# Kernel tuning notes

Hardware: AMD Instinct MI355X
Metric: run time of the kernel (lower is better)

The kernel has to match this reference:

```python
import jax, jax.numpy as jnp
import numpy as np

B, H, K, T, OUT, NH = 512, 512, 6, 60, 2, 8

def _gelu(x):
    return jax.nn.gelu(x, approximate=False)  # torch nn.GELU default = exact erf

def _layernorm(x, g, b, eps=1e-5):
    m = jnp.mean(x, axis=-1, keepdims=True)
    v = jnp.var(x, axis=-1, keepdims=True)
    return (x - m) * jax.lax.rsqrt(v + eps) * g + b

def setup_inputs() -> dict:
    key = jax.random.key(0)
    ks = iter(jax.random.split(key, 40))
    def p(shape, scale=0.02):
        return jax.random.normal(next(ks), shape, dtype=jnp.float32) * scale
    return dict(
        interaction_ctx=p((B, H), 1.0),
        cooperative_ctx=p((B, H), 1.0),
        map_ctx=p((B, H), 1.0),
        mode_queries=p((K, H)),
        # context_proj: Linear(3H,H) -> GELU -> Linear(H,H)
        Wc1=p((3 * H, H)), bc1=jnp.zeros((H,), jnp.float32),
        Wc2=p((H, H)), bc2=jnp.zeros((H,), jnp.float32),
        # coarse_heads stacked over modes: Linear(H,2H)->GELU->Linear(2H,T*OUT)
        Wk1=p((K, H, 2 * H)), bk1=jnp.zeros((K, 2 * H), jnp.float32),
        Wk2=p((K, 2 * H, T * OUT)), bk2=jnp.zeros((K, T * OUT), jnp.float32),
        # traj_encoder: Linear(OUT,H)->GELU
        Wt=p((OUT, H)), bt=jnp.zeros((H,), jnp.float32),
        # refine_attn (MultiheadAttention) projections
        Wq_a=p((H, H)), bq_a=jnp.zeros((H,), jnp.float32),
        Wk_a=p((H, H)), bk_a=jnp.zeros((H,), jnp.float32),
        Wv_a=p((H, H)), bv_a=jnp.zeros((H,), jnp.float32),
        Wo_a=p((H, H)), bo_a=jnp.zeros((H,), jnp.float32),
        ln_g=jnp.ones((H,), jnp.float32), ln_b=jnp.zeros((H,), jnp.float32),
        # refine_heads stacked over modes: Linear(H,H)->GELU->Linear(H,OUT)
        Wr1=p((K, H, H)), br1=jnp.zeros((K, H), jnp.float32),
        Wr2=p((K, H, OUT)), br2=jnp.zeros((K, OUT), jnp.float32),
        # conf_head: Linear(H,64)->ReLU->Linear(64,1)
        Wf1=p((H, 64)), bf1=jnp.zeros((64,), jnp.float32),
        Wf2=p((64, 1)), bf2=jnp.zeros((1,), jnp.float32),
    )

def reference(interaction_ctx, cooperative_ctx, map_ctx, mode_queries,
              Wc1, bc1, Wc2, bc2, Wk1, bk1, Wk2, bk2, Wt, bt,
              Wq_a, bq_a, Wk_a, bk_a, Wv_a, bv_a, Wo_a, bo_a,
              ln_g, ln_b, Wr1, br1, Wr2, br2, Wf1, bf1, Wf2, bf2):
    # dropout layers are identity in eval mode
    combined = jnp.concatenate([interaction_ctx, cooperative_ctx, map_ctx], axis=-1)  # (B,3H)
    context = _gelu(combined @ Wc1 + bc1) @ Wc2 + bc2                                 # (B,H)
    mode_features = mode_queries[None, :, :] + context[:, None, :]                    # (B,K,H)

    # coarse heads: per-mode loop -> grouped GEMM over mode axis
    h = _gelu(jnp.einsum('bkh,khf->bkf', mode_features, Wk1) + bk1)                   # (B,K,2H)
    coarse = (jnp.einsum('bkf,kfo->bko', h, Wk2) + bk2).reshape(B, K, T, OUT)          # (B,K,T,OUT)

    traj_feats = _gelu(coarse @ Wt + bt)                                              # (B,K,T,H)

    # refine_attn: keys/values are context broadcast over T (all identical), so
    # softmax weights are exactly uniform and attention output == out_proj(v_ctx).
    # (grads through Wq_a/Wk_a are exactly zero for the same reason.)
    v = context @ Wv_a + bv_a                                                         # (B,H)
    attn_out = v @ Wo_a + bo_a                                                        # (B,H)

    refined_feats = _layernorm(traj_feats + attn_out[:, None, None, :], ln_g, ln_b)   # (B,K,T,H)

    # refine heads: grouped GEMM over mode axis
    r = _gelu(jnp.einsum('bkth,khf->bktf', refined_feats, Wr1) + br1[:, None, :])     # (B,K,T,H)
    offsets = jnp.einsum('bktf,kfo->bkto', r, Wr2) + br2[:, None, :]                  # (B,K,T,OUT)
    predictions = coarse + offsets

    conf = jax.nn.relu(mode_features @ Wf1 + bf1) @ Wf2 + bf2                         # (B,K,1)
    mode_probs = jax.nn.softmax(conf[..., 0], axis=-1)                                # (B,K)
    return predictions, mode_probs
```

## Files before the change

### kernel.cpp

```cpp
#include <hip/hip_runtime.h>
#include <math.h>

#define BB 512
#define HH 512
#define KK 6
#define TT 60
#define OO 2
#define H2 1024
#define TO 120
#define RFP 520
#define HSP 1032

typedef __bf16 bf16x8 __attribute__((ext_vector_type(8)));
typedef float  f32x4  __attribute__((ext_vector_type(4)));
typedef float  f32x16 __attribute__((ext_vector_type(16)));

__device__ __forceinline__ float bf2f(unsigned short u) {
    union { unsigned int i; float f; } v; v.i = ((unsigned int)u) << 16; return v.f;
}
__device__ __forceinline__ unsigned short f2bf(float f) {
    union { float f; unsigned int i; } v; v.f = f;
    unsigned int b = v.i;
    return (unsigned short)((b + 0x7FFFu + ((b >> 16) & 1u)) >> 16);
}
__device__ __forceinline__ unsigned int pack2bf(float a, float b) {
    union { __bf16 h[2]; unsigned int u; } v;
    v.h[0] = (__bf16)a; v.h[1] = (__bf16)b;
    return v.u;
}
__device__ __forceinline__ float gelu_exact(float x) {
    return 0.5f * x * (1.0f + erff(x * 0.70710678118654752f));
}

#if defined(__has_builtin)
#  if __has_builtin(__builtin_amdgcn_rcpf)
#    define FAST_RCP(x) __builtin_amdgcn_rcpf(x)
#  endif
#  if __has_builtin(__builtin_amdgcn_exp2f)
#    define FAST_EXP2(x) __builtin_amdgcn_exp2f(x)
#  endif
#endif
#ifndef FAST_RCP
#  define FAST_RCP(x) (1.0f / (x))
#endif
#ifndef FAST_EXP2
#  define FAST_EXP2(x) __expf((x) * 0.69314718056f)
#endif

__device__ __forceinline__ float gelu_cheap(float x) {
    float x2 = x * x;
    float z = x * fmaf(0.10294324f, x2, 2.3022082f);
    float e = FAST_EXP2(-z);
    return x * FAST_RCP(1.0f + e);
}

struct F8 { float v[8]; };
__device__ __forceinline__ F8 load8f(const float* p) {
    F8 r;
    float4 a = *(const float4*)p;
    float4 b = *(const float4*)(p + 4);
    r.v[0] = a.x; r.v[1] = a.y; r.v[2] = a.z; r.v[3] = a.w;
    r.v[4] = b.x; r.v[5] = b.y; r.v[6] = b.z; r.v[7] = b.w;
    return r;
}
__device__ __forceinline__ F8 load8b(const unsigned short* p) {
    ushort4 a = *(const ushort4*)p;
    ushort4 b = *(const ushort4*)(p + 4);
    F8 r;
    r.v[0] = bf2f(a.x); r.v[1] = bf2f(a.y); r.v[2] = bf2f(a.z); r.v[3] = bf2f(a.w);
    r.v[4] = bf2f(b.x); r.v[5] = bf2f(b.y); r.v[6] = bf2f(b.z); r.v[7] = bf2f(b.w);
    return r;
}

struct PKD { const float* src; unsigned short* dst; int F, N, NC, nch, steps, Z; };
struct PK8 { PKD e[8]; };

__global__ void k_pack(PK8 d) {
    int rid = blockIdx.x * 4 + (threadIdx.x >> 6);
    const int ln = threadIdx.x & 63;
    int i = 0;
    while (i < 7) {
        int tot = d.e[i].Z * d.e[i].nch * d.e[i].steps;
        if (rid < tot) break;
        rid -= tot; ++i;
    }
    const PKD e = d.e[i];
    const int per = e.nch * e.steps;
    const int z = rid / per;
    const int r = rid - z * per;
    const int nch = r / e.steps, step = r - nch * e.steps;
    const float* src = e.src + (size_t)z * e.F * e.N;
    unsigned short* dst = e.dst + ((size_t)z * per + r) * 512 + ln * 8;
    int f_base, n;
    if (e.NC == 16) { f_base = step * 32 + (ln >> 4) * 8; n = nch * 16 + (ln & 15); }
    else            { f_base = step * 16 + (ln >> 5) * 8; n = nch * 32 + (ln & 31); }
    if (n >= e.N) n = e.N - 1;
    unsigned int pk[4];
#pragma unroll
    for (int j = 0; j < 4; ++j) {
        unsigned short lo = f2bf(src[(size_t)(f_base + 2 * j) * e.N + n]);
        unsigned short hi = f2bf(src[(size_t)(f_base + 2 * j + 1) * e.N + n]);
        pk[j] = (unsigned int)lo | ((unsigned int)hi << 16);
    }
    *(uint4*)dst = make_uint4(pk[0], pk[1], pk[2], pk[3]);
}

template <bool CONCAT, bool GELU>
__launch_bounds__(256)
__global__ void k_gemm_m(const void* __restrict__ A0, const void* __restrict__ A1,
                         const void* __restrict__ A2, const unsigned short* __restrict__ BP,
                         const float* __restrict__ bias, unsigned short* __restrict__ C,
                         int Kd) {
    __shared__ __align__(16) unsigned short As[32 * RFP];
    const int tid = threadIdx.x;
    const int bm = blockIdx.x * 32;
    const int bn = blockIdx.y * 64;
    const int w = tid >> 6, ln = tid & 63;
    const int lane15 = ln & 15, quad = ln >> 4;
    const int n = bn + w * 16 + lane15;
    const int nchunks = Kd / HH;
    const int stepsTot = Kd / 32;
    const int nchB = blockIdx.y * 4 + w;

    f32x4 acc0 = {0.f, 0.f, 0.f, 0.f}, acc1 = {0.f, 0.f, 0.f, 0.f};

    for (int kc = 0; kc < nchunks; ++kc) {
        {
            int r = tid >> 3, c0 = (tid & 7) * 64;
            unsigned short* dp = As + r * RFP + c0;
            if (CONCAT) {
                const float* src = (kc == 0) ? (const float*)A0
                                 : (kc == 1) ? (const float*)A1 : (const float*)A2;
                const float* sp = src + (bm + r) * HH + c0;
                for (int c = 0; c < 64; c += 8) {
                    F8 v = load8f(sp + c);
                    unsigned int pk[4];
#pragma unroll
                    for (int j = 0; j < 4; ++j)
                        pk[j] = pack2bf(v.v[2 * j], v.v[2 * j + 1]);
                    *(uint4*)(dp + c) = make_uint4(pk[0], pk[1], pk[2], pk[3]);
                }
            } else {
                const unsigned short* sp = (const unsigned short*)A0 + (bm + r) * HH + c0;
                for (int c = 0; c < 64; c += 8)
                    *(uint4*)(dp + c) = *(const uint4*)(sp + c);
            }
        }
        __syncthreads();
        const unsigned short* bp = BP + ((size_t)nchB * stepsTot + kc * 16) * 512 + ln * 8;
#pragma unroll
        for (int f0 = 0; f0 < HH; f0 += 32) {
            bf16x8 a0 = *(const bf16x8*)(As + lane15 * RFP + f0 + quad * 8);
            bf16x8 a1 = *(const bf16x8*)(As + (16 + lane15) * RFP + f0 + quad * 8);
            bf16x8 bf = *(const bf16x8*)(bp);
            bp += 512;
            acc0 = __builtin_amdgcn_mfma_f32_16x16x32_bf16(a0, bf, acc0, 0, 0, 0);
            acc1 = __builtin_amdgcn_mfma_f32_16x16x32_bf16(a1, bf, acc1, 0, 0, 0);
        }
        __syncthreads();
    }
    const float bb = bias[n];
#pragma unroll
    for (int reg = 0; reg < 4; ++reg) {
        float v0 = acc0[reg] + bb, v1 = acc1[reg] + bb;
        if (GELU) { v0 = gelu_exact(v0); v1 = gelu_exact(v1); }
        C[(bm + quad * 4 + reg) * HH + n] = f2bf(v0);
        C[(bm + 16 + quad * 4 + reg) * HH + n] = f2bf(v1);
    }
}

__launch_bounds__(512)
__global__ void k_bc(const unsigned short* __restrict__ ctx, const float* __restrict__ mq,
                     const unsigned short* __restrict__ Wk1P, const float* __restrict__ bk1,
                     const unsigned short* __restrict__ Wk2P, const float* __restrict__ bk2,
                     const unsigned short* __restrict__ Wf1P, const float* __restrict__ bf1,
                     const float* __restrict__ Wf2, const float* __restrict__ bf2v,
                     unsigned short* __restrict__ coarse_out, float* __restrict__ conf_out)
{
    __shared__ __align__(16) unsigned short mf[16 * RFP];
    __shared__ __align__(16) unsigned short hs[16 * HSP];

    const int tid = threadIdx.x;
    const int k = blockIdx.x % KK;
    const int b0 = (blockIdx.x / KK) * 16;
    const int w = tid >> 6;
    const int ln = tid & 63;
    const int lane15 = ln & 15;
    const int quad = ln >> 4;

    {
        int r = tid >> 5;
        int c0 = (tid & 31) * 16;
        const unsigned short* cp = ctx + (b0 + r) * HH + c0;
        const float* qp = mq + k * HH + c0;
        unsigned short* dp = mf + r * RFP + c0;
        for (int c = 0; c < 16; c += 8) {
            F8 cv = load8b(cp + c);
            F8 qv = load8f(qp + c);
            unsigned int pk[4];
#pragma unroll
            for (int j = 0; j < 4; ++j)
                pk[j] = pack2bf(cv.v[2 * j] + qv.v[2 * j], cv.v[2 * j + 1] + qv.v[2 * j + 1]);
            *(uint4*)(dp + c) = make_uint4(pk[0], pk[1], pk[2], pk[3]);
        }
    }
    __syncthreads();

    {
        const unsigned short* wk1p = Wk1P + (size_t)k * (64 * 16 * 512);
        const float* bk1p = bk1 + k * H2;
        for (int g = 0; g < 8; ++g) {
            const int n = w * 128 + g * 16 + lane15;
            f32x4 acc0 = {0.f,0.f,0.f,0.f};
            const unsigned short* bp = wk1p + (size_t)((w * 8 + g) * 16) * 512 + ln * 8;
#pragma unroll
            for (int f0 = 0; f0 < HH; f0 += 32) {
                bf16x8 a0 = *(const bf16x8*)(mf + lane15 * RFP + f0 + quad * 8);
                bf16x8 bf = *(const bf16x8*)(bp);
                bp += 512;
                acc0 = __builtin_amdgcn_mfma_f32_16x16x32_bf16(a0, bf, acc0, 0, 0, 0);
            }
            const float bias = bk1p[n];
#pragma unroll
            for (int reg = 0; reg < 4; ++reg)
                hs[(quad * 4 + reg) * HSP + n] = f2bf(gelu_exact(acc0[reg] + bias));
        }
    }
    __syncthreads();

    {
        const unsigned short* wk2p = Wk2P + (size_t)k * (8 * 32 * 512);
        const int n = w * 16 + lane15;
        f32x4 acc0 = {0.f,0.f,0.f,0.f};
        const unsigned short* bp = wk2p + (size_t)(w * 32) * 512 + ln * 8;
#pragma unroll
        for (int f0 = 0; f0 < H2; f0 += 32) {
            bf16x8 a0 = *(const bf16x8*)(hs + lane15 * HSP + f0 + quad * 8);
            bf16x8 bf = *(const bf16x8*)(bp);
            bp += 512;
            acc0 = __builtin_amdgcn_mfma_f32_16x16x32_bf16(a0, bf, acc0, 0, 0, 0);
        }
        if (n < TO) {
            const float bias = bk2[k * TO + n];
#pragma unroll
            for (int reg = 0; reg < 4; ++reg)
                coarse_out[((b0 + quad * 4 + reg) * KK + k) * TO + n] = f2bf(acc0[reg] + bias);
        }
    }

    if (w == 0) {
        f32x4 acc[4];
#pragma unroll
        for (int nt = 0; nt < 4; ++nt) { f32x4 z = {0.f,0.f,0.f,0.f}; acc[nt] = z; }
#pragma unroll
        for (int f0 = 0; f0 < HH; f0 += 32) {
            const int step = f0 >> 5;
            bf16x8 a0 = *(const bf16x8*)(mf + lane15 * RFP + f0 + quad * 8);
#pragma unroll
            for (int nt = 0; nt < 4; ++nt) {
                bf16x8 bf = *(const bf16x8*)(Wf1P + (size_t)(nt * 16 + step) * 512 + ln * 8);
                acc[nt] = __builtin_amdgcn_mfma_f32_16x16x32_bf16(a0, bf, acc[nt], 0, 0, 0);
            }
        }
        const float b2 = bf2v[0];
#pragma unroll
        for (int reg = 0; reg < 4; ++reg) {
            float s = 0.f;
#pragma unroll
            for (int nt = 0; nt < 4; ++nt) {
                const int n = nt * 16 + lane15;
                s = fmaf(fmaxf(acc[nt][reg] + bf1[n], 0.f), Wf2[n], s);
            }
#pragma unroll
            for (int off = 1; off < 16; off <<= 1) s += __shfl_xor(s, off);
            if (lane15 == 0)
                conf_out[(b0 + quad * 4 + reg) * KK + k] = s + b2;
        }
    }
}

__launch_bounds__(512, 4)
__global__ void k_ef(
    const unsigned short* __restrict__ attn, const unsigned short* __restrict__ coarse_ws,
    const float* __restrict__ Wt,  const float* __restrict__ bt,
    const float* __restrict__ lng, const float* __restrict__ lnb,
    const unsigned short* __restrict__ Wr1P, const float* __restrict__ br1,
    const float* __restrict__ Wr2, const float* __restrict__ br2,
    float* __restrict__ pred_out)
{
    __shared__ __align__(16) unsigned short rf[64 * RFP];
    __shared__ float coarse[TO];
    __shared__ float br1s[HH];
    __shared__ float2 wr2s[HH];
    __shared__ float po2[8][64][2];

    const int tid = threadIdx.x;
    const int b = blockIdx.x / KK;
    const int k = blockIdx.x % KK;
    const int w = tid >> 6;
    const int ln = tid & 63;
    const int lane31 = ln & 31;
    const int hf = ln >> 5;
    const int cbase = ln * 8;

    const unsigned short* attb = attn + b * HH;

    if (tid < TO) coarse[tid] = bf2f(coarse_ws[(b * KK + k) * TO + tid]);
    br1s[tid] = br1[k * HH + tid];
    wr2s[tid] = ((const float2*)Wr2)[(size_t)k * HH + tid];
    __syncthreads();

    {
        F8 w0 = load8f(Wt + cbase);
        F8 w1 = load8f(Wt + HH + cbase);
        F8 b8 = load8f(bt + cbase);
        F8 g8 = load8f(lng + cbase);
        F8 bb8 = load8f(lnb + cbase);
        F8 a8 = load8b(attb + cbase);
#pragma unroll
        for (int r = 0; r < 8; ++r) {
            int t = w + 8 * r;
            if (t < 60) {
                float co0 = coarse[2 * t], co1 = coarse[2 * t + 1];
                float x[8]; float s = 0.f, s2 = 0.f;
#pragma unroll
                for (int j = 0; j < 8; ++j) {
                    float vv = fmaf(co0, w0.v[j], fmaf(co1, w1.v[j], b8.v[j]));
                    vv = gelu_cheap(vv) + a8.v[j];
                    x[j] = vv; s += vv; s2 = fmaf(vv, vv, s2);
                }
#pragma unroll
                for (int off = 32; off > 0; off >>= 1) {
                    s += __shfl_xor(s, off);
                    s2 += __shfl_xor(s2, off);
                }
                float mean = s * (1.0f / HH);
                float var = fmaf(-mean, mean, s2 * (1.0f / HH));
                float inv = rsqrtf(var + 1e-5f);
                unsigned int pk[4];
#pragma unroll
                for (int j = 0; j < 4; ++j) {
                    float y0 = fmaf((x[2 * j] - mean) * inv, g8.v[2 * j], bb8.v[2 * j]);
                    float y1 = fmaf((x[2 * j + 1] - mean) * inv, g8.v[2 * j + 1], bb8.v[2 * j + 1]);
                    pk[j] = pack2bf(y0, y1);
                }
                *(uint4*)(rf + t * RFP + cbase) = make_uint4(pk[0], pk[1], pk[2], pk[3]);
            } else {
                *(uint4*)(rf + t * RFP + cbase) = make_uint4(0, 0, 0, 0);
            }
        }
    }
    __syncthreads();

    {
        const unsigned short* bp0 = Wr1P + (size_t)k * (16 * 32 * 512)
                                  + (size_t)(w * 2) * 32 * 512 + ln * 8;
        const unsigned short* bp1 = bp0 + 32 * 512;
        const int n0 = w * 64;
        const unsigned short* a0p = rf + lane31 * RFP + hf * 8;
        const unsigned short* a1p = a0p + 32 * RFP;

        f32x16 acc00 = {0.f,0.f,0.f,0.f,0.f,0.f,0.f,0.f,0.f,0.f,0.f,0.f,0.f,0.f,0.f,0.f};
        f32x16 acc01 = acc00, acc10 = acc00, acc11 = acc00;

        __builtin_amdgcn_s_setprio(1);
#pragma unroll
        for (int st = 0; st < 32; ++st) {
            const int k0 = st * 16;
            bf16x8 A0 = *(const bf16x8*)(a0p + k0);
            bf16x8 A1 = *(const bf16x8*)(a1p + k0);
            bf16x8 B0 = *(const bf16x8*)(bp0 + st * 512);
            bf16x8 B1 = *(const bf16x8*)(bp1 + st * 512);
            acc00 = __builtin_amdgcn_mfma_f32_32x32x16_bf16(B0, A0, acc00, 0, 0, 0);
            acc01 = __builtin_amdgcn_mfma_f32_32x32x16_bf16(B1, A0, acc01, 0, 0, 0);
            acc10 = __builtin_amdgcn_mfma_f32_32x32x16_bf16(B0, A1, acc10, 0, 0, 0);
            acc11 = __builtin_amdgcn_mfma_f32_32x32x16_bf16(B1, A1, acc11, 0, 0, 0);
        }
        __builtin_amdgcn_s_setprio(0);

        float p00 = 0.f, p01 = 0.f, p10 = 0.f, p11 = 0.f;
#pragma unroll
        for (int nt = 0; nt < 2; ++nt) {
#pragma unroll
            for (int reg = 0; reg < 16; ++reg) {
                const int n = n0 + nt * 32 + (reg & 3) + 8 * (reg >> 2) + 4 * hf;
                const float bb = br1s[n];
                const float2 w2 = wr2s[n];
                const float a0v = nt ? acc01[reg] : acc00[reg];
                const float a1v = nt ? acc11[reg] : acc10[reg];
                const float rv0 = gelu_cheap(a0v + bb);
                const float rv1 = gelu_cheap(a1v + bb);
                p00 = fmaf(rv0, w2.x, p00);
                p01 = fmaf(rv0, w2.y, p01);
                p10 = fmaf(rv1, w2.x, p10);
                p11 = fmaf(rv1, w2.y, p11);
            }
        }
        p00 += __shfl_xor(p00, 32);
        p01 += __shfl_xor(p01, 32);
        p10 += __shfl_xor(p10, 32);
        p11 += __shfl_xor(p11, 32);
        if (ln < 32) {
            *(float2*)&po2[w][lane31][0]      = make_float2(p00, p01);
            *(float2*)&po2[w][32 + lane31][0] = make_float2(p10, p11);
        }
    }
    __syncthreads();

    if (tid < TO) {
        int t = tid >> 1, o = tid & 1;
        float s = 0.f;
#pragma unroll
        for (int ww = 0; ww < 8; ++ww) s += po2[ww][t][o];
        pred_out[((b * KK + k) * TT + t) * 2 + o] = coarse[tid] + s + br2[k * 2 + o];
    }
}

__global__ void k_softmax(const float* __restrict__ conf, float* __restrict__ out) {
    int b = blockIdx.x * blockDim.x + threadIdx.x;
    if (b < BB) {
        float v[KK];
        float m = -1e30f;
        for (int i = 0; i < KK; ++i) { v[i] = conf[b * KK + i]; m = fmaxf(m, v[i]); }
        float s = 0.f;
        for (int i = 0; i < KK; ++i) { v[i] = __expf(v[i] - m); s += v[i]; }
        float inv = 1.0f / s;
        for (int i = 0; i < KK; ++i) out[b * KK + i] = v[i] * inv;
    }
}

extern "C" void kernel_launch(void* const* d_in, const int* in_sizes, int n_in,
                              void* d_out, int out_size, void* d_ws, size_t ws_size,
                              hipStream_t stream) {
    const float* I0  = (const float*)d_in[0];
    const float* I1  = (const float*)d_in[1];
    const float* I2  = (const float*)d_in[2];
    const float* MQ  = (const float*)d_in[3];
    const float* Wc1 = (const float*)d_in[4];
    const float* bc1 = (const float*)d_in[5];
    const float* Wc2 = (const float*)d_in[6];
    const float* bc2 = (const float*)d_in[7];
    const float* Wk1 = (const float*)d_in[8];
    const float* bk1 = (const float*)d_in[9];
    const float* Wk2 = (const float*)d_in[10];
    const float* bk2 = (const float*)d_in[11];
    const float* Wt  = (const float*)d_in[12];
    const float* bt  = (const float*)d_in[13];
    const float* Wv  = (const float*)d_in[18];
    const float* bv  = (const float*)d_in[19];
    const float* Wo  = (const float*)d_in[20];
    const float* bo  = (const float*)d_in[21];
    const float* lng = (const float*)d_in[22];
    const float* lnb = (const float*)d_in[23];
    const float* Wr1 = (const float*)d_in[24];
    const float* br1 = (const float*)d_in[25];
    const float* Wr2 = (const float*)d_in[26];
    const float* br2 = (const float*)d_in[27];
    const float* Wf1 = (const float*)d_in[28];
    const float* bf1 = (const float*)d_in[29];
    const float* Wf2 = (const float*)d_in[30];
    const float* bf2v = (const float*)d_in[31];

    unsigned short* wsu   = (unsigned short*)d_ws;
    unsigned short* wc1p  = wsu;
    unsigned short* wc2p  = wsu + 786432;
    unsigned short* wvp   = wsu + 1048576;
    unsigned short* wop   = wsu + 1310720;
    unsigned short* wk1p  = wsu + 1572864;
    unsigned short* wk2p  = wsu + 4718592;
    unsigned short* wf1p  = wsu + 5505024;
    unsigned short* wr1p  = wsu + 5537792;
    unsigned short* ctx   = wsu + 7110656;
    unsigned short* attn  = wsu + 7372800;
    unsigned short* tmp   = wsu + 7634944;
    unsigned short* coarse= wsu + 7897088;
    float* conf = (float*)(wsu + 8265728);

    float* pred = (float*)d_out;
    float* probs = pred + BB * KK * TT * OO;

    PK8 pk;
    pk.e[0] = {Wc1, wc1p, 3 * HH, HH, 16, 32, 48, 1};
    pk.e[1] = {Wc2, wc2p, HH, HH, 16, 32, 16, 1};
    pk.e[2] = {Wv,  wvp,  HH, HH, 16, 32, 16, 1};
    pk.e[3] = {Wo,  wop,  HH, HH, 16, 32, 16, 1};
    pk.e[4] = {Wk1, wk1p, HH, H2, 16, 64, 16, KK};
    pk.e[5] = {Wk2, wk2p, H2, TO, 16, 8, 32, KK};
    pk.e[6] = {Wf1, wf1p, HH, 64, 16, 4, 16, 1};
    pk.e[7] = {Wr1, wr1p, HH, HH, 32, 16, 32, KK};
    k_pack<<<dim3(3472), 256, 0, stream>>>(pk);

    k_gemm_m<true,  true ><<<dim3(16, 8), 256, 0, stream>>>(I0, I1, I2, wc1p, bc1, tmp, 3 * HH);
    k_gemm_m<false, false><<<dim3(16, 8), 256, 0, stream>>>(tmp, nullptr, nullptr, wc2p, bc2, ctx, HH);
    k_gemm_m<false, false><<<dim3(16, 8), 256, 0, stream>>>(ctx, nullptr, nullptr, wvp, bv, tmp, HH);
    k_gemm_m<false, false><<<dim3(16, 8), 256, 0, stream>>>(tmp, nullptr, nullptr, wop, bo, attn, HH);

    k_bc<<<dim3(192), 512, 0, stream>>>(ctx, MQ, wk1p, bk1, wk2p, bk2, wf1p, bf1, Wf2, bf2v,
                                        coarse, conf);
    k_ef<<<dim3(BB * KK), 512, 0, stream>>>(attn, coarse, Wt, bt, lng, lnb,
                                            wr1p, br1, Wr2, br2, pred);
    k_softmax<<<dim3(2), 256, 0, stream>>>(conf, probs);
}
```

Measured before the change: 330.7 us.

## Halve GEMM tile width, fuse V-projection into coarse-head kernel, fold softmax into refine

```diff
diff --git a/kernel.cpp b/kernel.cpp
--- a/kernel.cpp
+++ b/kernel.cpp
@@ -114,15 +114,17 @@
     __shared__ __align__(16) unsigned short As[32 * RFP];
     const int tid = threadIdx.x;
     const int bm = blockIdx.x * 32;
-    const int bn = blockIdx.y * 64;
+    const int bn = blockIdx.y * 32;
     const int w = tid >> 6, ln = tid & 63;
     const int lane15 = ln & 15, quad = ln >> 4;
-    const int n = bn + w * 16 + lane15;
+    const int mh = w >> 1;
+    const int ng = w & 1;
+    const int n = bn + ng * 16 + lane15;
     const int nchunks = Kd / HH;
     const int stepsTot = Kd / 32;
-    const int nchB = blockIdx.y * 4 + w;
-
-    f32x4 acc0 = {0.f, 0.f, 0.f, 0.f}, acc1 = {0.f, 0.f, 0.f, 0.f};
+    const int nchB = blockIdx.y * 2 + ng;
+
+    f32x4 acc0 = {0.f, 0.f, 0.f, 0.f};
 
     for (int kc = 0; kc < nchunks; ++kc) {
         {
@@ -150,43 +152,79 @@
         const unsigned short* bp = BP + ((size_t)nchB * stepsTot + kc * 16) * 512 + ln * 8;
 #pragma unroll
         for (int f0 = 0; f0 < HH; f0 += 32) {
-            bf16x8 a0 = *(const bf16x8*)(As + lane15 * RFP + f0 + quad * 8);
-            bf16x8 a1 = *(const bf16x8*)(As + (16 + lane15) * RFP + f0 + quad * 8);
+            bf16x8 a0 = *(const bf16x8*)(As + (mh * 16 + lane15) * RFP + f0 + quad * 8);
             bf16x8 bf = *(const bf16x8*)(bp);
             bp += 512;
             acc0 = __builtin_amdgcn_mfma_f32_16x16x32_bf16(a0, bf, acc0, 0, 0, 0);
-            acc1 = __builtin_amdgcn_mfma_f32_16x16x32_bf16(a1, bf, acc1, 0, 0, 0);
         }
         __syncthreads();
     }
     const float bb = bias[n];
 #pragma unroll
     for (int reg = 0; reg < 4; ++reg) {
-        float v0 = acc0[reg] + bb, v1 = acc1[reg] + bb;
-        if (GELU) { v0 = gelu_exact(v0); v1 = gelu_exact(v1); }
-        C[(bm + quad * 4 + reg) * HH + n] = f2bf(v0);
-        C[(bm + 16 + quad * 4 + reg) * HH + n] = f2bf(v1);
+        float v0 = acc0[reg] + bb;
+        if (GELU) v0 = gelu_exact(v0);
+        C[(bm + mh * 16 + quad * 4 + reg) * HH + n] = f2bf(v0);
     }
 }
 
 __launch_bounds__(512)
-__global__ void k_bc(const unsigned short* __restrict__ ctx, const float* __restrict__ mq,
-                     const unsigned short* __restrict__ Wk1P, const float* __restrict__ bk1,
-                     const unsigned short* __restrict__ Wk2P, const float* __restrict__ bk2,
-                     const unsigned short* __restrict__ Wf1P, const float* __restrict__ bf1,
-                     const float* __restrict__ Wf2, const float* __restrict__ bf2v,
-                     unsigned short* __restrict__ coarse_out, float* __restrict__ conf_out)
+__global__ void k_bcg(const unsigned short* __restrict__ ctx, const float* __restrict__ mq,
+                      const unsigned short* __restrict__ Wk1P, const float* __restrict__ bk1,
+                      const unsigned short* __restrict__ Wk2P, const float* __restrict__ bk2,
+                      const unsigned short* __restrict__ Wf1P, const float* __restrict__ bf1,
+                      const float* __restrict__ Wf2, const float* __restrict__ bf2v,
+                      unsigned short* __restrict__ coarse_out, float* __restrict__ conf_out,
+                      const unsigned short* __restrict__ WvP, const float* __restrict__ bv,
+                      unsigned short* __restrict__ vout)
 {
-    __shared__ __align__(16) unsigned short mf[16 * RFP];
-    __shared__ __align__(16) unsigned short hs[16 * HSP];
+    __shared__ __align__(16) unsigned short shbuf[24832];
 
     const int tid = threadIdx.x;
-    const int k = blockIdx.x % KK;
-    const int b0 = (blockIdx.x / KK) * 16;
     const int w = tid >> 6;
     const int ln = tid & 63;
     const int lane15 = ln & 15;
     const int quad = ln >> 4;
+
+    if (blockIdx.x >= 192) {
+        unsigned short* As = shbuf;
+        const int gbid = blockIdx.x - 192;
+        const int bm = (gbid & 15) * 32;
+        const int gy = gbid >> 4;
+        const int bn = gy * 64;
+        const int mh = w >> 2;
+        const int ng = w & 3;
+        const int n = bn + ng * 16 + lane15;
+        const int nchB = gy * 4 + ng;
+
+        {
+            int r = tid >> 4, c0 = (tid & 15) * 32;
+            const unsigned short* sp = ctx + (bm + r) * HH + c0;
+            unsigned short* dp = As + r * RFP + c0;
+            for (int c = 0; c < 32; c += 8)
+                *(uint4*)(dp + c) = *(const uint4*)(sp + c);
+        }
+        __syncthreads();
+        f32x4 acc0 = {0.f, 0.f, 0.f, 0.f};
+        const unsigned short* bp = WvP + (size_t)nchB * 16 * 512 + ln * 8;
+#pragma unroll
+        for (int f0 = 0; f0 < HH; f0 += 32) {
+            bf16x8 a0 = *(const bf16x8*)(As + (mh * 16 + lane15) * RFP + f0 + quad * 8);
+            bf16x8 bf = *(const bf16x8*)(bp);
+            bp += 512;
+            acc0 = __builtin_amdgcn_mfma_f32_16x16x32_bf16(a0, bf, acc0, 0, 0, 0);
+        }
+        const float bb = bv[n];
+#pragma unroll
+        for (int reg = 0; reg < 4; ++reg)
+            vout[(bm + mh * 16 + quad * 4 + reg) * HH + n] = f2bf(acc0[reg] + bb);
+        return;
+    }
+
+    unsigned short* mf = shbuf;
+    unsigned short* hs = shbuf + 16 * RFP;
+    const int k = blockIdx.x % KK;
+    const int b0 = (blockIdx.x / KK) * 16;
 
     {
         int r = tid >> 5;
@@ -286,7 +324,8 @@
     const float* __restrict__ lng, const float* __restrict__ lnb,
     const unsigned short* __restrict__ Wr1P, const float* __restrict__ br1,
     const float* __restrict__ Wr2, const float* __restrict__ br2,
-    float* __restrict__ pred_out)
+    float* __restrict__ pred_out,
+    const float* __restrict__ conf, float* __restrict__ probs)
 {
     __shared__ __align__(16) unsigned short rf[64 * RFP];
     __shared__ float coarse[TO];
@@ -308,6 +347,18 @@
     if (tid < TO) coarse[tid] = bf2f(coarse_ws[(b * KK + k) * TO + tid]);
     br1s[tid] = br1[k * HH + tid];
     wr2s[tid] = ((const float2*)Wr2)[(size_t)k * HH + tid];
+
+    if (k == 0 && tid == 448) {
+        float v[KK]; float m = -1e30f;
+#pragma unroll
+        for (int i = 0; i < KK; ++i) { v[i] = conf[b * KK + i]; m = fmaxf(m, v[i]); }
+        float s = 0.f;
+#pragma unroll
+        for (int i = 0; i < KK; ++i) { v[i] = __expf(v[i] - m); s += v[i]; }
+        float inv = 1.0f / s;
+#pragma unroll
+        for (int i = 0; i < KK; ++i) probs[b * KK + i] = v[i] * inv;
+    }
     __syncthreads();
 
     {
@@ -413,19 +464,6 @@
 #pragma unroll
         for (int ww = 0; ww < 8; ++ww) s += po2[ww][t][o];
         pred_out[((b * KK + k) * TT + t) * 2 + o] = coarse[tid] + s + br2[k * 2 + o];
-    }
-}
-
-__global__ void k_softmax(const float* __restrict__ conf, float* __restrict__ out) {
-    int b = blockIdx.x * blockDim.x + threadIdx.x;
-    if (b < BB) {
-        float v[KK];
-        float m = -1e30f;
-        for (int i = 0; i < KK; ++i) { v[i] = conf[b * KK + i]; m = fmaxf(m, v[i]); }
-        float s = 0.f;
-        for (int i = 0; i < KK; ++i) { v[i] = __expf(v[i] - m); s += v[i]; }
-        float inv = 1.0f / s;
-        for (int i = 0; i < KK; ++i) out[b * KK + i] = v[i] * inv;
     }
 }
 
@@ -490,14 +528,14 @@
     pk.e[7] = {Wr1, wr1p, HH, HH, 32, 16, 32, KK};
     k_pack<<<dim3(3472), 256, 0, stream>>>(pk);
 
-    k_gemm_m<true,  true ><<<dim3(16, 8), 256, 0, stream>>>(I0, I1, I2, wc1p, bc1, tmp, 3 * HH);
-    k_gemm_m<false, false><<<dim3(16, 8), 256, 0, stream>>>(tmp, nullptr, nullptr, wc2p, bc2, ctx, HH);
-    k_gemm_m<false, false><<<dim3(16, 8), 256, 0, stream>>>(ctx, nullptr, nullptr, wvp, bv, tmp, HH);
-    k_gemm_m<false, false><<<dim3(16, 8), 256, 0, stream>>>(tmp, nullptr, nullptr, wop, bo, attn, HH);
-
-    k_bc<<<dim3(192), 512, 0, stream>>>(ctx, MQ, wk1p, bk1, wk2p, bk2, wf1p, bf1, Wf2, bf2v,
-                                        coarse, conf);
+    k_gemm_m<true,  true ><<<dim3(16, 16), 256, 0, stream>>>(I0, I1, I2, wc1p, bc1, tmp, 3 * HH);
+    k_gemm_m<false, false><<<dim3(16, 16), 256, 0, stream>>>(tmp, nullptr, nullptr, wc2p, bc2, ctx, HH);
+
+    k_bcg<<<dim3(320), 512, 0, stream>>>(ctx, MQ, wk1p, bk1, wk2p, bk2, wf1p, bf1, Wf2, bf2v,
+                                         coarse, conf, wvp, bv, tmp);
+
+    k_gemm_m<false, false><<<dim3(16, 16), 256, 0, stream>>>(tmp, nullptr, nullptr, wop, bo, attn, HH);
+
     k_ef<<<dim3(BB * KK), 512, 0, stream>>>(attn, coarse, Wt, bt, lng, lnb,
-                                            wr1p, br1, Wr2, br2, pred);
-    k_softmax<<<dim3(2), 256, 0, stream>>>(conf, probs);
-}
+                                            wr1p, br1, Wr2, br2, pred, conf, probs);
+}
```

Result: no change. 324.8 us (-1.8%).
